# Kernel optimization log

Hardware: AMD Instinct MI355X
Metric: run time of the kernel (lower is better)

## Reference

```python
import jax, jax.numpy as jnp
import numpy as np

B, N, D = 8, 1024, 256
H = 8
DH = D // H
R = 4          # relation types 0..3; adj value 4 = no relation
FF = 1024
EPS = 1e-5


def _lin(k, fan_in, shape):
    return jax.random.normal(k, shape, jnp.float32) * (1.0 / np.sqrt(fan_in))


def setup_inputs() -> dict:
    key = jax.random.key(0)
    ks = jax.random.split(key, 16)
    src = jax.random.normal(ks[0], (B, N, D), jnp.float32)
    adj_matrix = jax.random.randint(ks[1], (B, N, N), 0, 5, dtype=jnp.int32)
    Wq = _lin(ks[2], D, (D, D)); bq = jnp.zeros((D,), jnp.float32)
    Wk = _lin(ks[3], D, (D, D)); bk = jnp.zeros((D,), jnp.float32)
    Wv = _lin(ks[4], D, (R, D, D)); bv = jnp.zeros((R, D), jnp.float32)
    Wo = _lin(ks[5], D, (D, D)); bo = jnp.zeros((D,), jnp.float32)
    W1 = _lin(ks[6], D, (D, FF)); b1 = jnp.zeros((FF,), jnp.float32)
    W2 = _lin(ks[7], FF, (FF, D)); b2 = jnp.zeros((D,), jnp.float32)
    g1 = jnp.ones((D,), jnp.float32); beta1 = jnp.zeros((D,), jnp.float32)
    g2 = jnp.ones((D,), jnp.float32); beta2 = jnp.zeros((D,), jnp.float32)
    return dict(src=src, adj_matrix=adj_matrix, Wq=Wq, bq=bq, Wk=Wk, bk=bk,
                Wv=Wv, bv=bv, Wo=Wo, bo=bo, W1=W1, b1=b1, W2=W2, b2=b2,
                g1=g1, beta1=beta1, g2=g2, beta2=beta2)


def _ln(x, g, b):
    m = x.mean(-1, keepdims=True)
    v = ((x - m) ** 2).mean(-1, keepdims=True)
    return (x - m) * jax.lax.rsqrt(v + EPS) * g + b


def reference(src, adj_matrix, Wq, bq, Wk, bk, Wv, bv, Wo, bo, W1, b1, W2, b2, g1, beta1, g2, beta2):
    Bb, Nn, Dm = src.shape
    h, dh = H, Dm // H
    q = (src @ Wq + bq).reshape(Bb, Nn, h, dh).transpose(0, 2, 1, 3)  # (B,H,N,dh)
    k = (src @ Wk + bk).reshape(Bb, Nn, h, dh).transpose(0, 2, 1, 3)
    scores = jnp.einsum('bhid,bhjd->bhij', q, k) / np.sqrt(dh)
    attn = jax.nn.softmax(scores, axis=-1)                             # (B,H,N,N)
    out = jnp.zeros_like(q)
    for r in range(Wv.shape[0]):  # small fixed relation loop, matches module
        v_r = (src @ Wv[r] + bv[r]).reshape(Bb, Nn, h, dh).transpose(0, 2, 1, 3)
        mask = (adj_matrix == r)[:, None]                              # (B,1,N,N)
        out = out + jnp.einsum('bhij,bhjd->bhid', attn * mask, v_r)
    attn_out = out.transpose(0, 2, 1, 3).reshape(Bb, Nn, Dm) @ Wo + bo
    x = _ln(src + attn_out, g1, beta1)
    ff = jax.nn.gelu(x @ W1 + b1, approximate=False) @ W2 + b2
    return _ln(x + ff, g2, beta2)
```

## Files before the change

### kernel.cpp

```cpp
#include <hip/hip_runtime.h>
#include <hip/hip_bf16.h>
#include <cmath>

constexpr int CB  = 8;
constexpr int CN  = 1024;
constexpr int CD  = 256;
constexpr int CH  = 8;
constexpr int CDH = 32;
constexpr int CR  = 4;
constexpr int CFF = 1024;
constexpr float CEPS = 1e-5f;
constexpr float CS = 0.25503480f;
constexpr size_t SZH = (size_t)CB * CH * CN * CDH;

#define MODE_QK    0
#define MODE_FFN1  2
#define MODE_VT    4

typedef float v4f __attribute__((ext_vector_type(4)));
typedef short v8s __attribute__((ext_vector_type(8)));

static __device__ __forceinline__ short f2bf(float f) {
    unsigned u = __builtin_bit_cast(unsigned, f);
    u += 0x7fff + ((u >> 16) & 1);
    return (short)(u >> 16);
}
static __device__ __forceinline__ float bf2f(short s) {
    unsigned u = ((unsigned)(unsigned short)s) << 16;
    return __builtin_bit_cast(float, u);
}
static __device__ __forceinline__ unsigned cvtpk_bf16(float lo, float hi) {
    unsigned r;
    asm("v_cvt_pk_bf16_f32 %0, %1, %2" : "=v"(r) : "v"(lo), "v"(hi));
    return r;
}

static __device__ __forceinline__ void async_copy16(const void* g, void* l) {
    __builtin_amdgcn_global_load_lds(
        (const __attribute__((address_space(1))) void*)g,
        (__attribute__((address_space(3))) void*)l, 16, 0, 0);
}


template<int BM, int BN, int MODE>
__device__ __forceinline__ void gemm_body(
    const short* __restrict__ A, const short* __restrict__ Bw,
    const float* __restrict__ biasv, void* __restrict__ dest,
    int M, int K, int Nw, int bx, int by, short* smem)
{
    constexpr int WTM = BM / 2, WTN = BN / 2;
    constexpr int TM = WTM / 16, TN = WTN / 16;
    short* As = smem;
    short* Bs = smem + 2 * BM * 32;

    const int t    = threadIdx.x;
    const int lane = t & 63;
    const int w    = t >> 6;
    const int quad = lane >> 4, l15 = lane & 15;
    const int wm = w >> 1, wn = w & 1;
    const int m0 = bx * BM, n0 = by * BN;

    const int srow = lane >> 2;
    const int scol = (lane & 3) * 8;

    v4f acc[TM][TN];
    #pragma unroll
    for (int i = 0; i < TM; ++i)
        #pragma unroll
        for (int j = 0; j < TN; ++j) acc[i][j] = (v4f){0.f, 0.f, 0.f, 0.f};

    const int NK = K >> 5;

    auto stage = [&](int buf, int kt) {
        #pragma unroll
        for (int u = 0; u < BM / 64; ++u) {
            const int e0 = (w * (BM / 64) + u) * 512;
            const int row = (e0 >> 5) + srow;
            async_copy16(A + (size_t)(m0 + row) * K + kt + scol,
                         &As[buf * BM * 32 + e0]);
        }
        #pragma unroll
        for (int u = 0; u < BN / 64; ++u) {
            const int e0 = (w * (BN / 64) + u) * 512;
            const int row = (e0 >> 5) + srow;
            async_copy16(Bw + (size_t)(n0 + row) * K + kt + scol,
                         &Bs[buf * BN * 32 + e0]);
        }
    };

    stage(0, 0);

    for (int it = 0; it < NK; ++it) {
        __syncthreads();
        if (it + 1 < NK) stage((it + 1) & 1, (it + 1) << 5);

        const int buf = it & 1;
        v8s af[TM], bfr[TN];
        #pragma unroll
        for (int i = 0; i < TM; ++i)
            af[i] = *(const v8s*)&As[buf * BM * 32 +
                                     (wm * WTM + i * 16 + l15) * 32 + quad * 8];
        #pragma unroll
        for (int j = 0; j < TN; ++j)
            bfr[j] = *(const v8s*)&Bs[buf * BN * 32 +
                                      (wn * WTN + j * 16 + l15) * 32 + quad * 8];
        #pragma unroll
        for (int i = 0; i < TM; ++i)
            #pragma unroll
            for (int j = 0; j < TN; ++j)
                acc[i][j] = __builtin_amdgcn_mfma_f32_16x16x32_bf16(
                    af[i], bfr[j], acc[i][j], 0, 0, 0);
    }

    #pragma unroll
    for (int i = 0; i < TM; ++i) {
        #pragma unroll
        for (int j = 0; j < TN; ++j) {
            const int mb = m0 + wm * WTM + i * 16 + quad * 4;
            const int n  = n0 + wn * WTN + j * 16 + l15;
            float vals[4];
            if (MODE == MODE_VT) {
                #pragma unroll
                for (int rr = 0; rr < 4; ++rr) vals[rr] = acc[i][j][rr] + biasv[mb + rr];
            } else {
                #pragma unroll
                for (int rr = 0; rr < 4; ++rr) vals[rr] = acc[i][j][rr] + biasv[n];
            }

            if (MODE == MODE_QK) {
                if (n0 < 256) {
                    #pragma unroll
                    for (int rr = 0; rr < 4; ++rr) vals[rr] *= CS;
                }
                const int b = mb >> 10, ii0 = mb & 1023;
                const int plane = n >> 8, nn = n & 255;
                const int h = nn >> 5, d = nn & 31;
                #pragma unroll
                for (int rr = 0; rr < 4; ++rr)
                    ((short*)dest)[(size_t)plane * SZH +
                        (((size_t)(b * CH + h)) * CN + ii0 + rr) * CDH + d] =
                        f2bf(vals[rr]);
            } else if (MODE == MODE_VT) {
                const int b = n >> 10, ii = n & 1023;
                const int jj = ii & 63;
                const int cc = (((jj >> 4) & 1) << 5) | (((jj >> 2) & 3) << 3) |
                               (((jj >> 5) & 1) << 2) | (jj & 3);
                const int iip = (ii & ~63) | cc;
                #pragma unroll
                for (int rr = 0; rr < 4; ++rr) {
                    const int m = mb + rr;
                    const int r2 = m >> 8, hd = m & 255;
                    const int h = hd >> 5, d = hd & 31;
                    ((short*)dest)[2 * SZH +
                        (((size_t)(r2 * 64 + b * CH + h)) * CDH + d) * CN + iip] =
                        f2bf(vals[rr]);
                }
            } else {
                #pragma unroll
                for (int rr = 0; rr < 4; ++rr) {
                    const size_t idx = (size_t)(mb + rr) * Nw + n;
                    const float xx = vals[rr];
                    const float E = exp2f(2.302217f * (xx + 0.044715f * xx * xx * xx));
                    ((short*)dest)[idx] = f2bf(xx * E / (E + 1.f));
                }
            }
        }
    }
}

template<int BM, int BN, int MODE>
__global__ __launch_bounds__(256)
void gemm_mfma(const short* __restrict__ A, const short* __restrict__ Bw,
               const float* __restrict__ biasv, void* __restrict__ dest,
               int M, int K, int Nw)
{
    extern __shared__ short smem[];
    gemm_body<BM, BN, MODE>(A, Bw, biasv, dest, M, K, Nw,
                            blockIdx.x, blockIdx.y, smem);
}

__global__ __launch_bounds__(256)
void proj_kernel(const short* __restrict__ src_bf, const short* __restrict__ wqkvT,
                 const float* __restrict__ bpack, short* __restrict__ qkv,
                 const int* __restrict__ adj, unsigned char* __restrict__ adjsel)
{
    extern __shared__ short smem[];
    const int g = blockIdx.x;
    if (g < 256) {
        gemm_body<128, 128, MODE_QK>(src_bf, wqkvT, bpack, qkv,
                                     8192, 256, 512, g >> 2, g & 3, smem);
    } else if (g < 768) {
        const int h2 = g - 256;
        gemm_body<128, 128, MODE_VT>(wqkvT + 512 * 256, src_bf, bpack + 512,
                                     qkv, 1024, 256, 8192, h2 & 7, h2 >> 3, smem);
    } else {
        const int nout = CB * CN * CN / 8;
        for (int i = (g - 768) * 256 + threadIdx.x; i < nout; i += 512 * 256) {
            const int dwi = i & 127;
            const int row = i >> 7;
            const int T   = dwi >> 3, kq = dwi & 7;
            const int j0  = T * 64 + (kq & 3) * 4 + (kq >> 2) * 16;
            const int* p = adj + (size_t)row * CN + j0;
            const int4 q0 = *(const int4*)(p);
            const int4 q1 = *(const int4*)(p + 32);
            int2 o;
            o.x = (q0.x & 0xff) | ((q0.y & 0xff) << 8) |
                  ((q0.z & 0xff) << 16) | ((q0.w & 0xff) << 24);
            o.y = (q1.x & 0xff) | ((q1.y & 0xff) << 8) |
                  ((q1.z & 0xff) << 16) | ((q1.w & 0xff) << 24);
            ((int2*)adjsel)[i] = o;
        }
    }
}

template<bool OUTF, bool OUTB, bool ADDBF>
__global__ __launch_bounds__(256)
void gemm_ln32(const short* __restrict__ A, const short* __restrict__ Bw,
               const float* __restrict__ biasv, const void* __restrict__ addp,
               const float* __restrict__ gw, const float* __restrict__ be,
               float* __restrict__ outf, short* __restrict__ outb, int K)
{
    __shared__ short As[2][16 * 64];
    __shared__ short Bs[2][256 * 64];
    __shared__ float redS[16][4], redQ[16][4];

    const int t    = threadIdx.x;
    const int lane = t & 63;
    const int w    = t >> 6;
    const int quad = lane >> 4, l15 = lane & 15;
    const int m0   = blockIdx.x * 16;
    const int xsw  = l15 & 7;

    v4f acc[4];
    #pragma unroll
    for (int j = 0; j < 4; ++j) acc[j] = (v4f){0.f, 0.f, 0.f, 0.f};

    const int NK = K >> 6;

    auto stage = [&](int buf, int kt) {
        if (t < 128) {
            const int row = t >> 3, gc = t & 7;
            async_copy16(A + (size_t)(m0 + row) * K + kt + ((gc ^ (row & 7)) * 8),
                         &As[buf][t * 8]);
        }
        #pragma unroll
        for (int u = 0; u < 8; ++u) {
            const int gl = t + 256 * u;
            const int row = gl >> 3, gc = gl & 7;
            async_copy16(Bw + (size_t)row * K + kt + ((gc ^ (row & 7)) * 8),
                         &Bs[buf][gl * 8]);
        }
    };

    stage(0, 0);

    for (int it = 0; it < NK; ++it) {
        __syncthreads();
        if (it + 1 < NK) stage((it + 1) & 1, (it + 1) << 6);

        const int buf = it & 1;
        #pragma unroll
        for (int half = 0; half < 2; ++half) {
            const int gr = (quad + 4 * half) ^ xsw;
            const v8s af = *(const v8s*)&As[buf][l15 * 64 + gr * 8];
            #pragma unroll
            for (int j = 0; j < 4; ++j) {
                const v8s bfr = *(const v8s*)&Bs[buf][(w * 64 + 16 * j + l15) * 64 + gr * 8];
                acc[j] = __builtin_amdgcn_mfma_f32_16x16x32_bf16(af, bfr, acc[j], 0, 0, 0);
            }
        }
    }

    float v[4][4];
    #pragma unroll
    for (int rr = 0; rr < 4; ++rr) {
        const int row = m0 + quad * 4 + rr;
        float s = 0.f, sq = 0.f;
        #pragma unroll
        for (int j = 0; j < 4; ++j) {
            const int n = w * 64 + 16 * j + l15;
            const size_t idx = (size_t)row * CD + n;
            const float addv = ADDBF ? bf2f(((const short*)addp)[idx])
                                     : ((const float*)addp)[idx];
            const float x = acc[j][rr] + biasv[n] + addv;
            v[rr][j] = x;
            s += x; sq += x * x;
        }
        #pragma unroll
        for (int off = 1; off < 16; off <<= 1) {
            s  += __shfl_xor(s, off);
            sq += __shfl_xor(sq, off);
        }
        if (l15 == 0) {
            redS[quad * 4 + rr][w] = s;
            redQ[quad * 4 + rr][w] = sq;
        }
    }
    __syncthreads();

    #pragma unroll
    for (int rr = 0; rr < 4; ++rr) {
        const int r16 = quad * 4 + rr;
        const int row = m0 + r16;
        const float s  = (redS[r16][0] + redS[r16][1]) + (redS[r16][2] + redS[r16][3]);
        const float sq = (redQ[r16][0] + redQ[r16][1]) + (redQ[r16][2] + redQ[r16][3]);
        const float mean = s * (1.f / CD);
        const float var  = sq * (1.f / CD) - mean * mean;
        const float rstd = rsqrtf(var + CEPS);
        #pragma unroll
        for (int j = 0; j < 4; ++j) {
            const int n = w * 64 + 16 * j + l15;
            const float y = (v[rr][j] - mean) * rstd * gw[n] + be[n];
            if (OUTF) outf[(size_t)row * CD + n] = y;
            if (OUTB) outb[(size_t)row * CD + n] = f2bf(y);
        }
    }
}

__global__ __launch_bounds__(256)
void prep(const float* __restrict__ src,
          const float* __restrict__ Wq, const float* __restrict__ Wk,
          const float* __restrict__ Wv, const float* __restrict__ Wo,
          const float* __restrict__ W1, const float* __restrict__ W2,
          const float* __restrict__ bq, const float* __restrict__ bk,
          const float* __restrict__ bv, const float* __restrict__ bo,
          const float* __restrict__ b1, const float* __restrict__ b2,
          short* __restrict__ src_bf,
          short* __restrict__ wqkvT, short* __restrict__ woT,
          short* __restrict__ w1T, short* __restrict__ w2T,
          float* __restrict__ bpack)
{
    __shared__ float tile[64][65];
    const int bx = blockIdx.x, t = threadIdx.x;
    if (bx < 2048) {
        const int i = bx * 256 + t;
        const float4 v = ((const float4*)src)[i];
        short4 o;
        o.x = f2bf(v.x); o.y = f2bf(v.y); o.z = f2bf(v.z); o.w = f2bf(v.w);
        ((short4*)src_bf)[i] = o;
    } else if (bx < 2288) {
        const int tt = bx - 2048;
        const float* S; short* D;
        int Sstride, Dstride, k0, srccol, dstrow;
        if (tt < 96) {
            const int tk = tt & 3, tn = tt >> 2;
            const int ng = tn * 64;
            Sstride = 256; Dstride = 256; k0 = tk * 64;
            dstrow = tn * 64; D = wqkvT;
            if (ng < 256)      { S = Wq; srccol = ng; }
            else if (ng < 512) { S = Wk; srccol = ng - 256; }
            else { const int r = (ng - 512) >> 8;
                   S = Wv + (size_t)r * 65536; srccol = (ng - 512) & 255; }
        } else if (tt < 112) {
            const int u = tt - 96, tk = u & 3, tn = u >> 2;
            S = Wo; Sstride = 256; D = woT; Dstride = 256;
            k0 = tk * 64; srccol = tn * 64; dstrow = tn * 64;
        } else if (tt < 176) {
            const int u = tt - 112, tk = u & 3, tn = u >> 2;
            S = W1; Sstride = 1024; D = w1T; Dstride = 256;
            k0 = tk * 64; srccol = tn * 64; dstrow = tn * 64;
        } else {
            const int u = tt - 176, tk = u & 15, tn = u >> 4;
            S = W2; Sstride = 256; D = w2T; Dstride = 1024;
            k0 = tk * 64; srccol = tn * 64; dstrow = tn * 64;
        }
        #pragma unroll
        for (int u2 = 0; u2 < 4; ++u2) {
            const int kl = (t >> 4) + u2 * 16;
            const int nl = (t & 15) * 4;
            const float4 v = *(const float4*)&S[(size_t)(k0 + kl) * Sstride + srccol + nl];
            tile[kl][nl + 0] = v.x; tile[kl][nl + 1] = v.y;
            tile[kl][nl + 2] = v.z; tile[kl][nl + 3] = v.w;
        }
        __syncthreads();
        #pragma unroll
        for (int u2 = 0; u2 < 4; ++u2) {
            const int nl = (t >> 4) + u2 * 16;
            const int kl = (t & 15) * 4;
            short4 o;
            o.x = f2bf(tile[kl + 0][nl]); o.y = f2bf(tile[kl + 1][nl]);
            o.z = f2bf(tile[kl + 2][nl]); o.w = f2bf(tile[kl + 3][nl]);
            *(short4*)&D[(size_t)(dstrow + nl) * Dstride + k0 + kl] = o;
        }
    } else {
        const int idx = (bx - 2288) * 256 + t;
        float bvv;
        if (idx < 256)       bvv = bq[idx];
        else if (idx < 512)  bvv = bk[idx - 256];
        else if (idx < 1536) bvv = bv[idx - 512];
        else if (idx < 1792) bvv = bo[idx - 1536];
        else if (idx < 2816) bvv = b1[idx - 1792];
        else                 bvv = b2[idx - 2816];
        bpack[idx] = bvv;
    }
}

__global__ __launch_bounds__(256, 2)
void attn_mfma(const short* __restrict__ qg, const short* __restrict__ kg,
               const short* __restrict__ vt, const unsigned char* __restrict__ adjsel,
               short* __restrict__ outh)
{
    __shared__ __align__(16) short vtl[2][8192];

    const int t    = threadIdx.x;
    const int lane = t & 63;
    const int w    = t >> 6;
    const int quad = lane >> 4;
    const int l15  = lane & 15;
    const int g    = blockIdx.x;
    const int b    = g & 7;
    const int h    = (g >> 3) & 7;
    const int i0   = (g >> 6) * 128;
    const int bhh  = b * CH + h;
    const size_t bh = (size_t)bhh;

    v8s qfrag[2];
    #pragma unroll
    for (int hh = 0; hh < 2; ++hh)
        qfrag[hh] = *(const v8s*)&qg[(bh * CN + i0 + 64 * hh + 16 * w + l15) * CDH + quad * 8];

    const short* vsrc[4];
    #pragma unroll
    for (int u = 0; u < 4; ++u) {
        const int gl = t + 256 * u;
        const int r = gl >> 8, d = (gl >> 3) & 31, gc = gl & 7;
        vsrc[u] = vt + ((size_t)(r * 64 + bhh) * CDH + d) * CN + (gc ^ (d & 7)) * 8;
    }
    const short* kbase = kg + (bh * CN + l15) * CDH + quad * 8;
    const unsigned char* abase[2];
    #pragma unroll
    for (int hh = 0; hh < 2; ++hh)
        abase[hh] = adjsel + ((size_t)(b * CN) + i0 + 64 * hh + 16 * w + l15) * CN + quad * 8;

    v4f oacc[2][2][2];
    #pragma unroll
    for (int hh = 0; hh < 2; ++hh)
        #pragma unroll
        for (int cb = 0; cb < 2; ++cb)
            #pragma unroll
            for (int kb = 0; kb < 2; ++kb) oacc[hh][cb][kb] = (v4f){0.f, 0.f, 0.f, 0.f};
    float plsum[2] = {0.f, 0.f};
    const int psw = (l15 & 7) * 8;

    #pragma unroll
    for (int u = 0; u < 4; ++u)
        async_copy16(vsrc[u], &vtl[0][(t + 256 * u) * 8]);
    v8s kpre[4];
    #pragma unroll
    for (int jb = 0; jb < 4; ++jb)
        kpre[jb] = *(const v8s*)(kbase + (16 * jb) * CDH);
    int2 apre[2][2];
    #pragma unroll
    for (int hh = 0; hh < 2; ++hh) {
        apre[hh][0] = *(const int2*)(abase[hh]);
        apre[hh][1] = *(const int2*)(abase[hh] + 32);
    }

    for (int jt = 0; jt < 16; ++jt) {
        __syncthreads();
        const int p = jt & 1;

        v4f sacc[2][4];
        #pragma unroll
        for (int hh = 0; hh < 2; ++hh)
            #pragma unroll
            for (int jb = 0; jb < 4; ++jb)
                sacc[hh][jb] = __builtin_amdgcn_mfma_f32_16x16x32_bf16(
                    kpre[jb], qfrag[hh], (v4f){0.f, 0.f, 0.f, 0.f}, 0, 0, 0);

        int2 aa[2][2];
        #pragma unroll
        for (int hh = 0; hh < 2; ++hh) {
            aa[hh][0] = apre[hh][0];
            aa[hh][1] = apre[hh][1];
        }
        const int jn = (jt + 1) & 15;
        #pragma unroll
        for (int u = 0; u < 4; ++u)
            async_copy16(vsrc[u] + jn * 64, &vtl[p ^ 1][(t + 256 * u) * 8]);
        #pragma unroll
        for (int jb = 0; jb < 4; ++jb)
            kpre[jb] = *(const v8s*)(kbase + (jn * 64 + 16 * jb) * CDH);
        #pragma unroll
        for (int hh = 0; hh < 2; ++hh) {
            apre[hh][0] = *(const int2*)(abase[hh] + jn * 64);
            apre[hh][1] = *(const int2*)(abase[hh] + jn * 64 + 32);
        }

        float pv[2][4][4];
        #pragma unroll
        for (int hh = 0; hh < 2; ++hh) {
            #pragma unroll
            for (int jb = 0; jb < 4; ++jb)
                #pragma unroll
                for (int rr = 0; rr < 4; ++rr) pv[hh][jb][rr] = exp2f(sacc[hh][jb][rr]);
            plsum[hh] += ((pv[hh][0][0] + pv[hh][0][1]) + (pv[hh][0][2] + pv[hh][0][3]))
                       + ((pv[hh][1][0] + pv[hh][1][1]) + (pv[hh][1][2] + pv[hh][1][3]))
                       + ((pv[hh][2][0] + pv[hh][2][1]) + (pv[hh][2][2] + pv[hh][2][3]))
                       + ((pv[hh][3][0] + pv[hh][3][1]) + (pv[hh][3][2] + pv[hh][3][3]));
        }

        #pragma unroll
        for (int kb = 0; kb < 2; ++kb) {
            v8s vf[4][2];
            #pragma unroll
            for (int r = 0; r < 4; ++r)
                #pragma unroll
                for (int cb = 0; cb < 2; ++cb)
                    vf[r][cb] = *(const v8s*)&vtl[p][r * 2048 +
                        (16 * cb + l15) * 64 + (((4 * kb + quad) * 8) ^ psw)];

            #pragma unroll
            for (int hh = 0; hh < 2; ++hh) {
                const unsigned P[4] = {
                    cvtpk_bf16(pv[hh][kb][0],     pv[hh][kb][1]),
                    cvtpk_bf16(pv[hh][kb][2],     pv[hh][kb][3]),
                    cvtpk_bf16(pv[hh][kb + 2][0], pv[hh][kb + 2][1]),
                    cvtpk_bf16(pv[hh][kb + 2][2], pv[hh][kb + 2][3])};
                const int2 a2 = aa[hh][kb];
                const unsigned D[4] = {
                    __builtin_amdgcn_perm((unsigned)a2.x, (unsigned)a2.x, 0x01010000u),
                    __builtin_amdgcn_perm((unsigned)a2.x, (unsigned)a2.x, 0x03030202u),
                    __builtin_amdgcn_perm((unsigned)a2.y, (unsigned)a2.y, 0x01010000u),
                    __builtin_amdgcn_perm((unsigned)a2.y, (unsigned)a2.y, 0x03030202u)};
                unsigned pfm[4][4];
                #pragma unroll
                for (int r = 0; r < 4; ++r) {
                    const unsigned tb = 0xffu << (8 * r);
                    #pragma unroll
                    for (int u = 0; u < 4; ++u)
                        pfm[r][u] = P[u] & __builtin_amdgcn_perm(0u, tb, D[u]);
                }
                __builtin_amdgcn_s_setprio(1);
                #pragma unroll
                for (int r = 0; r < 4; ++r) {
                    const v8s pfr = __builtin_bit_cast(v8s,
                        make_uint4(pfm[r][0], pfm[r][1], pfm[r][2], pfm[r][3]));
                    #pragma unroll
                    for (int cb = 0; cb < 2; ++cb)
                        oacc[hh][cb][kb] = __builtin_amdgcn_mfma_f32_16x16x32_bf16(
                            pfr, vf[r][cb], oacc[hh][cb][kb], 0, 0, 0);
                }
                __builtin_amdgcn_s_setprio(0);
            }
        }
    }

    #pragma unroll
    for (int hh = 0; hh < 2; ++hh) {
        v4f ofin[2];
        ofin[0] = oacc[hh][0][0] + oacc[hh][0][1];
        ofin[1] = oacc[hh][1][0] + oacc[hh][1][1];
        float plF = plsum[hh];
        plF += __shfl_xor(plF, 16);
        plF += __shfl_xor(plF, 32);
        #pragma unroll
        for (int rr = 0; rr < 4; ++rr) {
            const float inv = 1.f / __shfl(plF, quad * 4 + rr);
            const int row = i0 + 64 * hh + 16 * w + quad * 4 + rr;
            #pragma unroll
            for (int cb = 0; cb < 2; ++cb)
                outh[((size_t)b * CN + row) * CD + h * CDH + 16 * cb + l15] =
                    f2bf(ofin[cb][rr] * inv);
        }
    }
}

extern "C" void kernel_launch(void* const* d_in, const int* in_sizes, int n_in,
                              void* d_out, int out_size, void* d_ws, size_t ws_size,
                              hipStream_t stream)
{
    const float* src = (const float*)d_in[0];
    const int*   adj = (const int*)d_in[1];
    const float* Wq  = (const float*)d_in[2];
    const float* bq  = (const float*)d_in[3];
    const float* Wk  = (const float*)d_in[4];
    const float* bk  = (const float*)d_in[5];
    const float* Wv  = (const float*)d_in[6];
    const float* bv  = (const float*)d_in[7];
    const float* Wo  = (const float*)d_in[8];
    const float* bo  = (const float*)d_in[9];
    const float* W1  = (const float*)d_in[10];
    const float* b1  = (const float*)d_in[11];
    const float* W2  = (const float*)d_in[12];
    const float* b2  = (const float*)d_in[13];
    const float* g1  = (const float*)d_in[14];
    const float* be1 = (const float*)d_in[15];
    const float* g2  = (const float*)d_in[16];
    const float* be2 = (const float*)d_in[17];
    float* out = (float*)d_out;

    char* wsb = (char*)d_ws;
    const size_t MB = (size_t)1 << 20;

    unsigned char* adjsel = (unsigned char*)(wsb);
    short* qkv_bf = (short*)(wsb + 8 * MB);
    short* src_bf = (short*)(wsb + 32 * MB);
    short* wqkvT  = (short*)(wsb + 36 * MB);
    short* woT    = (short*)(wsb + 36 * MB + 768 * 1024);
    short* w1T    = (short*)(wsb + 36 * MB + 896 * 1024);
    short* w2T    = (short*)(wsb + 36 * MB + 1408 * 1024);
    float* bpack  = (float*)(wsb + 36 * MB + 1920 * 1024);
    short* heads_bf = (short*)(wsb + 38 * MB);
    short* x_bf   = (short*)(wsb + 32 * MB);
    short* h1_bf  = (short*)(wsb + 16 * MB);

    const int M = CB * CN;
    dim3 blk(256);

    prep<<<dim3(2300), blk, 0, stream>>>(src, Wq, Wk, Wv, Wo, W1, W2,
        bq, bk, bv, bo, b1, b2, src_bf, wqkvT, woT, w1T, w2T, bpack);

    proj_kernel<<<dim3(1280), blk, 32768, stream>>>(
        src_bf, wqkvT, bpack, qkv_bf, adj, adjsel);

    attn_mfma<<<dim3(512), blk, 0, stream>>>(
        qkv_bf, qkv_bf + SZH, qkv_bf + 2 * SZH, adjsel, heads_bf);

    gemm_ln32<false, true, false><<<dim3(M / 16), blk, 0, stream>>>(
        heads_bf, woT, bpack + 1536, src, g1, be1, nullptr, x_bf, CD);

    gemm_mfma<64, 128, MODE_FFN1><<<dim3(M / 64, CFF / 128), blk, 24576, stream>>>(
        x_bf, w1T, bpack + 1792, h1_bf, M, CD, CFF);

    gemm_ln32<true, false, true><<<dim3(M / 16), blk, 0, stream>>>(
        h1_bf, w2T, bpack + 2816, x_bf, g2, be2, out, nullptr, CFF);
}
```

Before: 210.4 us.

## Split attention over the key dimension into two halves with a merge kernel

The attention kernel gains a split-K mode in which each block processes half of the key tiles, doubling the grid from 512 to 1024 blocks. Each block writes unnormalized fp32 partial outputs and row sums to workspace, and a new merge kernel adds the two halves, normalizes, and writes the bf16 heads. The aim is better CU occupancy, since 512 blocks underfill the MI355X's 256 CUs at two blocks per CU. The cost is extra fp32 global traffic plus one more launch. It also relies on the softmax having no running max, so the partial sums can simply be added.

```diff
diff --git a/kernel.cpp b/kernel.cpp
--- a/kernel.cpp
+++ b/kernel.cpp
@@ -395,10 +395,12 @@
     }
 }
 
+template<int SPLIT>
 __global__ __launch_bounds__(256, 2)
 void attn_mfma(const short* __restrict__ qg, const short* __restrict__ kg,
                const short* __restrict__ vt, const unsigned char* __restrict__ adjsel,
-               short* __restrict__ outh)
+               short* __restrict__ outh, float* __restrict__ po,
+               float* __restrict__ pd)
 {
     __shared__ __align__(16) short vtl[2][8192];
 
@@ -408,11 +410,14 @@
     const int quad = lane >> 4;
     const int l15  = lane & 15;
     const int g    = blockIdx.x;
+    const int jhalf = SPLIT ? (g >> 9) : 0;
     const int b    = g & 7;
     const int h    = (g >> 3) & 7;
-    const int i0   = (g >> 6) * 128;
+    const int i0   = ((g >> 6) & 7) * 128;
     const int bhh  = b * CH + h;
     const size_t bh = (size_t)bhh;
+    const int jt0  = jhalf * 8;
+    const int NT   = SPLIT ? 8 : 16;
 
     v8s qfrag[2];
     #pragma unroll
@@ -444,21 +449,21 @@
 
     #pragma unroll
     for (int u = 0; u < 4; ++u)
-        async_copy16(vsrc[u], &vtl[0][(t + 256 * u) * 8]);
+        async_copy16(vsrc[u] + jt0 * 64, &vtl[0][(t + 256 * u) * 8]);
     v8s kpre[4];
     #pragma unroll
     for (int jb = 0; jb < 4; ++jb)
-        kpre[jb] = *(const v8s*)(kbase + (16 * jb) * CDH);
+        kpre[jb] = *(const v8s*)(kbase + (jt0 * 64 + 16 * jb) * CDH);
     int2 apre[2][2];
     #pragma unroll
     for (int hh = 0; hh < 2; ++hh) {
-        apre[hh][0] = *(const int2*)(abase[hh]);
-        apre[hh][1] = *(const int2*)(abase[hh] + 32);
-    }
-
-    for (int jt = 0; jt < 16; ++jt) {
+        apre[hh][0] = *(const int2*)(abase[hh] + jt0 * 64);
+        apre[hh][1] = *(const int2*)(abase[hh] + jt0 * 64 + 32);
+    }
+
+    for (int jt = jt0; jt < jt0 + NT; ++jt) {
         __syncthreads();
-        const int p = jt & 1;
+        const int p = (jt - jt0) & 1;
 
         v4f sacc[2][4];
         #pragma unroll
@@ -554,16 +559,52 @@
         float plF = plsum[hh];
         plF += __shfl_xor(plF, 16);
         plF += __shfl_xor(plF, 32);
-        #pragma unroll
-        for (int rr = 0; rr < 4; ++rr) {
-            const float inv = 1.f / __shfl(plF, quad * 4 + rr);
-            const int row = i0 + 64 * hh + 16 * w + quad * 4 + rr;
-            #pragma unroll
-            for (int cb = 0; cb < 2; ++cb)
-                outh[((size_t)b * CN + row) * CD + h * CDH + 16 * cb + l15] =
-                    f2bf(ofin[cb][rr] * inv);
-        }
-    }
+        if (SPLIT) {
+            if (quad == 0)
+                pd[((size_t)jhalf * 64 + bhh) * CN + (i0 + 64 * hh + 16 * w + l15)] = plF;
+            #pragma unroll
+            for (int rr = 0; rr < 4; ++rr) {
+                const int row = i0 + 64 * hh + 16 * w + quad * 4 + rr;
+                #pragma unroll
+                for (int cb = 0; cb < 2; ++cb)
+                    po[((size_t)jhalf * CB * CN + (size_t)b * CN + row) * CD +
+                       h * CDH + 16 * cb + l15] = ofin[cb][rr];
+            }
+        } else {
+            #pragma unroll
+            for (int rr = 0; rr < 4; ++rr) {
+                const float inv = 1.f / __shfl(plF, quad * 4 + rr);
+                const int row = i0 + 64 * hh + 16 * w + quad * 4 + rr;
+                #pragma unroll
+                for (int cb = 0; cb < 2; ++cb)
+                    outh[((size_t)b * CN + row) * CD + h * CDH + 16 * cb + l15] =
+                        f2bf(ofin[cb][rr] * inv);
+            }
+        }
+    }
+}
+
+__global__ __launch_bounds__(256)
+void attn_merge(const float* __restrict__ po, const float* __restrict__ pd,
+                short* __restrict__ outh)
+{
+    const int i4 = blockIdx.x * 256 + threadIdx.x;
+    const size_t e0 = (size_t)i4 * 4;
+    const float4 a = ((const float4*)po)[i4];
+    const float4 c = ((const float4*)(po + (size_t)CB * CN * CD))[i4];
+    const int n   = (int)(e0 & 255);
+    const int hh  = n >> 5;
+    const int row = (int)((e0 >> 8) & 1023);
+    const int bb  = (int)(e0 >> 18);
+    const int bh  = bb * CH + hh;
+    const float den = pd[(size_t)bh * CN + row] + pd[(size_t)(64 + bh) * CN + row];
+    const float inv = 1.f / den;
+    short4 o;
+    o.x = f2bf((a.x + c.x) * inv);
+    o.y = f2bf((a.y + c.y) * inv);
+    o.z = f2bf((a.z + c.z) * inv);
+    o.w = f2bf((a.w + c.w) * inv);
+    ((short4*)outh)[i4] = o;
 }
 
 extern "C" void kernel_launch(void* const* d_in, const int* in_sizes, int n_in,
@@ -604,9 +645,12 @@
     short* heads_bf = (short*)(wsb + 38 * MB);
     short* x_bf   = (short*)(wsb + 32 * MB);
     short* h1_bf  = (short*)(wsb + 16 * MB);
+    float* po     = (float*)(wsb + 42 * MB);
+    float* pd     = (float*)(wsb + 58 * MB);
 
     const int M = CB * CN;
     dim3 blk(256);
+    const bool split = ws_size >= 59 * MB;
 
     prep<<<dim3(2300), blk, 0, stream>>>(src, Wq, Wk, Wv, Wo, W1, W2,
         bq, bk, bv, bo, b1, b2, src_bf, wqkvT, woT, w1T, w2T, bpack);
@@ -614,8 +658,14 @@
     proj_kernel<<<dim3(1280), blk, 32768, stream>>>(
         src_bf, wqkvT, bpack, qkv_bf, adj, adjsel);
 
-    attn_mfma<<<dim3(512), blk, 0, stream>>>(
-        qkv_bf, qkv_bf + SZH, qkv_bf + 2 * SZH, adjsel, heads_bf);
+    if (split) {
+        attn_mfma<1><<<dim3(1024), blk, 0, stream>>>(
+            qkv_bf, qkv_bf + SZH, qkv_bf + 2 * SZH, adjsel, heads_bf, po, pd);
+        attn_merge<<<dim3(2048), blk, 0, stream>>>(po, pd, heads_bf);
+    } else {
+        attn_mfma<0><<<dim3(512), blk, 0, stream>>>(
+            qkv_bf, qkv_bf + SZH, qkv_bf + 2 * SZH, adjsel, heads_bf, po, pd);
+    }
 
     gemm_ln32<false, true, false><<<dim3(M / 16), blk, 0, stream>>>(
         heads_bf, woT, bpack + 1536, src, g1, be1, nullptr, x_bf, CD);
```

Result: slower. 218.2 us (+3.7%).
